# Kernel tuning notes

Hardware: AMD Instinct MI355X
Metric: run time of the kernel (lower is better)

Reference implementation:

```python
import jax, jax.numpy as jnp
import numpy as np

N_NODES = 50000
N_EDGES = 800000
IN_DIM = 512
HEADS = 4
OUT_DIM = 64


def setup_inputs() -> dict:
    key = jax.random.key(0)
    k1, k2, k3, k4 = jax.random.split(key, 4)
    x = jax.random.normal(k1, (N_NODES, IN_DIM), dtype=jnp.float32)
    edges = jax.random.randint(k2, (N_EDGES, 2), 0, N_NODES, dtype=jnp.int32)
    W = jax.random.normal(k3, (IN_DIM, HEADS * OUT_DIM), dtype=jnp.float32) * 0.05
    a = jax.random.normal(k4, (HEADS, 2 * OUT_DIM), dtype=jnp.float32) * 0.05
    bias = jnp.zeros((HEADS * OUT_DIM,), dtype=jnp.float32)
    return {"x": x, "edges": edges, "W": W, "a": a, "bias": bias}


def reference(x, edges, W, a, bias):
    num_nodes = x.shape[0]
    # project: [N, H, D]
    h = (x @ W).reshape(num_nodes, HEADS, OUT_DIM)
    src = edges[:, 0]
    dst = edges[:, 1]
    # raw attention per edge, per head: e = sum(a * concat(h_src, h_dst))
    a_src = a[:, :OUT_DIM]   # [H, D]
    a_dst = a[:, OUT_DIM:]   # [H, D]
    # precompute per-node dot-products, then gather (avoids [E,H,2D] concat)
    s_src = jnp.einsum('nhd,hd->nh', h, a_src)  # [N, H]
    s_dst = jnp.einsum('nhd,hd->nh', h, a_dst)  # [N, H]
    e = s_src[src] + s_dst[dst]                 # [E, H]
    e = jax.nn.leaky_relu(e, negative_slope=0.2)
    # softmax over edges grouped by SOURCE node (as in original code)
    max_e = jax.ops.segment_max(e, src, num_segments=num_nodes)  # [N, H]
    exp_e = jnp.exp(e - max_e[src])
    sum_exp = jax.ops.segment_sum(exp_e, src, num_segments=num_nodes)
    alpha = exp_e / (sum_exp[src] + 1e-10)       # [E, H]
    # messages aggregated at DESTINATION node
    messages = alpha[:, :, None] * h[src]        # [E, H, D]
    out = jax.ops.segment_sum(messages, dst, num_segments=num_nodes)  # [N, H, D]
    out = out.reshape(num_nodes, HEADS * OUT_DIM) + bias
    return out
```

## Files before the change

kernel.cpp:

```cpp
#include <hip/hip_runtime.h>
#include <math.h>

#define IN_DIM 512
#define NH 4
#define OD 64
#define HD 256

typedef float  floatx4 __attribute__((ext_vector_type(4)));
typedef short  shortx8 __attribute__((ext_vector_type(8)));

__device__ __forceinline__ unsigned short f2bf(float x) {
    unsigned int u = __float_as_uint(x);
    u += 0x7fffu + ((u >> 16) & 1u);
    return (unsigned short)(u >> 16);
}
__device__ __forceinline__ float bf2f(unsigned short u) {
    return __uint_as_float(((unsigned int)u) << 16);
}

__global__ void prep_kernel(const float* __restrict__ W, ushort* __restrict__ Wt,
                            int* __restrict__ head_src, int* __restrict__ head_dst,
                            int M) {
    int t = blockIdx.x * blockDim.x + threadIdx.x;
    if (t < 2 * M) head_src[t] = -1;
    if (t < 4 * M) head_dst[t] = -1;
    if (t < 256 * 64) {
        int n = t >> 6;
        int k8 = (t & 63) * 8;
        shortx8 v;
        #pragma unroll
        for (int j = 0; j < 8; ++j) v[j] = (short)f2bf(W[(size_t)(k8 + j) * HD + n]);
        *(shortx8*)&Wt[(size_t)n * IN_DIM + k8] = v;
    }
}

__global__ __launch_bounds__(256) void gemm_kernel(const float* __restrict__ x,
                                                   const ushort* __restrict__ Wt,
                                                   ushort* __restrict__ h,
                                                   const float* __restrict__ a,
                                                   float2* __restrict__ ssi,
                                                   float* __restrict__ s_dst,
                                                   int M) {
    __shared__ ushort As[64 * 64];
    __shared__ ushort Bs[256 * 64];
    const int tid = threadIdx.x;
    const int lane = tid & 63;
    const int w = tid >> 6;
    const int bm = blockIdx.x * 64;
    const int wn = w * 64;
    const int lm = lane & 15;
    const int lq = lane >> 4;
    floatx4 acc[4][4];
    #pragma unroll
    for (int i = 0; i < 4; ++i)
        #pragma unroll
        for (int j = 0; j < 4; ++j) acc[i][j] = (floatx4){0.f, 0.f, 0.f, 0.f};

    for (int k0 = 0; k0 < IN_DIM; k0 += 64) {
        #pragma unroll
        for (int j = 0; j < 2; ++j) {
            int ch = tid * 2 + j;
            int row = ch >> 3;
            int c = (ch & 7) ^ (row & 7);
            int gr = bm + row;
            shortx8 v = (shortx8){0, 0, 0, 0, 0, 0, 0, 0};
            if (gr < M) {
                const float* gp = &x[(size_t)gr * IN_DIM + k0 + c * 8];
                float4 v0 = *(const float4*)gp;
                float4 v1 = *(const float4*)(gp + 4);
                v[0] = (short)f2bf(v0.x); v[1] = (short)f2bf(v0.y);
                v[2] = (short)f2bf(v0.z); v[3] = (short)f2bf(v0.w);
                v[4] = (short)f2bf(v1.x); v[5] = (short)f2bf(v1.y);
                v[6] = (short)f2bf(v1.z); v[7] = (short)f2bf(v1.w);
            }
            *(shortx8*)&As[ch * 8] = v;
        }
        #pragma unroll
        for (int j = 0; j < 8; ++j) {
            int ch = j * 256 + tid;
            int row = ch >> 3;
            int c = (ch & 7) ^ (row & 7);
            const ushort* gp = &Wt[(size_t)row * IN_DIM + k0 + c * 8];
            __builtin_amdgcn_global_load_lds(
                (const __attribute__((address_space(1))) void*)gp,
                (__attribute__((address_space(3))) void*)&Bs[(size_t)(j * 256 + wn) * 8],
                16, 0, 0);
        }
        __syncthreads();
        #pragma unroll
        for (int kk = 0; kk < 2; ++kk) {
            shortx8 af[4], bfr[4];
            #pragma unroll
            for (int mt = 0; mt < 4; ++mt) {
                int row = mt * 16 + lm;
                int c = (kk * 4 + lq) ^ (row & 7);
                af[mt] = *(const shortx8*)&As[row * 64 + c * 8];
            }
            #pragma unroll
            for (int nt = 0; nt < 4; ++nt) {
                int row = wn + nt * 16 + lm;
                int c = (kk * 4 + lq) ^ (row & 7);
                bfr[nt] = *(const shortx8*)&Bs[row * 64 + c * 8];
            }
            #pragma unroll
            for (int mt = 0; mt < 4; ++mt)
                #pragma unroll
                for (int nt = 0; nt < 4; ++nt)
                    acc[mt][nt] = __builtin_amdgcn_mfma_f32_16x16x32_bf16(
                        af[mt], bfr[nt], acc[mt][nt], 0, 0, 0);
        }
        __syncthreads();
    }
    float as_l[4], ad_l[4];
    #pragma unroll
    for (int nt = 0; nt < 4; ++nt) {
        as_l[nt] = a[w * 2 * OD + nt * 16 + lm];
        ad_l[nt] = a[w * 2 * OD + OD + nt * 16 + lm];
    }
    #pragma unroll
    for (int mt = 0; mt < 4; ++mt)
        #pragma unroll
        for (int r = 0; r < 4; ++r) {
            float ps = 0.f, pd = 0.f;
            #pragma unroll
            for (int nt = 0; nt < 4; ++nt) {
                float v = acc[mt][nt][r];
                ps += v * as_l[nt];
                pd += v * ad_l[nt];
            }
            #pragma unroll
            for (int off = 1; off < 16; off <<= 1) {
                ps += __shfl_xor(ps, off, 64);
                pd += __shfl_xor(pd, off, 64);
            }
            int m = bm + mt * 16 + lq * 4 + r;
            if (m < M && lm == 0) {
                ssi[m * NH + w].x = ps;
                s_dst[m * NH + w] = pd;
            }
        }
    #pragma unroll
    for (int mt = 0; mt < 4; ++mt)
        #pragma unroll
        for (int r = 0; r < 4; ++r) {
            int m = bm + mt * 16 + lq * 4 + r;
            if (m < M) {
                #pragma unroll
                for (int nt = 0; nt < 4; ++nt)
                    h[(size_t)m * HD + wn + nt * 16 + lm] = f2bf(acc[mt][nt][r]);
            }
        }
}

__global__ void link_kernel(const int2* __restrict__ edges,
                            int* __restrict__ head_src, int2* __restrict__ next_src,
                            int* __restrict__ head_dst, int2* __restrict__ next_dst,
                            int E) {
    int i = blockIdx.x * blockDim.x + threadIdx.x;
    if (i >= E) return;
    int2 e = edges[i];
    int ps = atomicExch(&head_src[2 * e.x + (i & 1)], i);
    next_src[i] = make_int2(ps, e.y);
    int pd = atomicExch(&head_dst[4 * e.y + (i & 3)], i);
    next_dst[i] = make_int2(pd, e.x);
}

__global__ void src_sum_kernel(const int* __restrict__ head_src,
                               const int2* __restrict__ next_src,
                               float2* __restrict__ ssi,
                               const float* __restrict__ s_dst, int M) {
    int n = blockIdx.x * blockDim.x + threadIdx.x;
    if (n >= M) return;
    float ss0 = ssi[n * NH + 0].x, ss1 = ssi[n * NH + 1].x;
    float ss2 = ssi[n * NH + 2].x, ss3 = ssi[n * NH + 3].x;
    float4 sum = make_float4(0.f, 0.f, 0.f, 0.f);
    int e0 = head_src[2 * n], e1 = head_src[2 * n + 1];
    while (e0 != -1 || e1 != -1) {
        if (e0 != -1) {
            int2 t = next_src[e0];
            float4 sd = *(const float4*)&s_dst[t.y * NH];
            float a0 = ss0 + sd.x, a1 = ss1 + sd.y, a2 = ss2 + sd.z, a3 = ss3 + sd.w;
            a0 = a0 > 0.f ? a0 : 0.2f * a0;
            a1 = a1 > 0.f ? a1 : 0.2f * a1;
            a2 = a2 > 0.f ? a2 : 0.2f * a2;
            a3 = a3 > 0.f ? a3 : 0.2f * a3;
            sum.x += __expf(a0); sum.y += __expf(a1);
            sum.z += __expf(a2); sum.w += __expf(a3);
            e0 = t.x;
        }
        if (e1 != -1) {
            int2 t = next_src[e1];
            float4 sd = *(const float4*)&s_dst[t.y * NH];
            float a0 = ss0 + sd.x, a1 = ss1 + sd.y, a2 = ss2 + sd.z, a3 = ss3 + sd.w;
            a0 = a0 > 0.f ? a0 : 0.2f * a0;
            a1 = a1 > 0.f ? a1 : 0.2f * a1;
            a2 = a2 > 0.f ? a2 : 0.2f * a2;
            a3 = a3 > 0.f ? a3 : 0.2f * a3;
            sum.x += __expf(a0); sum.y += __expf(a1);
            sum.z += __expf(a2); sum.w += __expf(a3);
            e1 = t.x;
        }
    }
    ssi[n * NH + 0].y = 1.f / (sum.x + 1e-10f);
    ssi[n * NH + 1].y = 1.f / (sum.y + 1e-10f);
    ssi[n * NH + 2].y = 1.f / (sum.z + 1e-10f);
    ssi[n * NH + 3].y = 1.f / (sum.w + 1e-10f);
}

__global__ void gather_kernel(const int* __restrict__ head_dst,
                              const int2* __restrict__ next_dst,
                              const float2* __restrict__ ssi,
                              const float* __restrict__ s_dst,
                              const ushort* __restrict__ h,
                              const float* __restrict__ bias,
                              float* __restrict__ out, int M) {
    int lane = threadIdx.x & 63;
    int n = blockIdx.x * 4 + (threadIdx.x >> 6);
    if (n >= M) return;
    int half = lane >> 5;
    int l5 = lane & 31;
    int head = l5 >> 3;
    int c0 = l5 * 8;
    float sdst = s_dst[n * NH + head];
    floatx4 accA = {0.f, 0.f, 0.f, 0.f}, accB = {0.f, 0.f, 0.f, 0.f};
    int e0 = head_dst[4 * n + 2 * half];
    int e1 = head_dst[4 * n + 2 * half + 1];
    while (e0 != -1 || e1 != -1) {
        if (e0 != -1) {
            int2 t = next_dst[e0];
            int src = t.y;
            float2 si = ssi[src * NH + head];
            float es = si.x + sdst;
            es = es > 0.f ? es : 0.2f * es;
            float al = __expf(es) * si.y;
            shortx8 hu = *(const shortx8*)&h[(size_t)src * HD + c0];
            accA.x += al * bf2f((ushort)hu[0]); accA.y += al * bf2f((ushort)hu[1]);
            accA.z += al * bf2f((ushort)hu[2]); accA.w += al * bf2f((ushort)hu[3]);
            accB.x += al * bf2f((ushort)hu[4]); accB.y += al * bf2f((ushort)hu[5]);
            accB.z += al * bf2f((ushort)hu[6]); accB.w += al * bf2f((ushort)hu[7]);
            e0 = t.x;
        }
        if (e1 != -1) {
            int2 t = next_dst[e1];
            int src = t.y;
            float2 si = ssi[src * NH + head];
            float es = si.x + sdst;
            es = es > 0.f ? es : 0.2f * es;
            float al = __expf(es) * si.y;
            shortx8 hu = *(const shortx8*)&h[(size_t)src * HD + c0];
            accA.x += al * bf2f((ushort)hu[0]); accA.y += al * bf2f((ushort)hu[1]);
            accA.z += al * bf2f((ushort)hu[2]); accA.w += al * bf2f((ushort)hu[3]);
            accB.x += al * bf2f((ushort)hu[4]); accB.y += al * bf2f((ushort)hu[5]);
            accB.z += al * bf2f((ushort)hu[6]); accB.w += al * bf2f((ushort)hu[7]);
            e1 = t.x;
        }
    }
    accA.x += __shfl_xor(accA.x, 32, 64); accA.y += __shfl_xor(accA.y, 32, 64);
    accA.z += __shfl_xor(accA.z, 32, 64); accA.w += __shfl_xor(accA.w, 32, 64);
    accB.x += __shfl_xor(accB.x, 32, 64); accB.y += __shfl_xor(accB.y, 32, 64);
    accB.z += __shfl_xor(accB.z, 32, 64); accB.w += __shfl_xor(accB.w, 32, 64);
    if (half == 0) {
        float4 b0 = *(const float4*)&bias[c0];
        float4 b1 = *(const float4*)&bias[c0 + 4];
        float4 o0 = make_float4(accA.x + b0.x, accA.y + b0.y, accA.z + b0.z, accA.w + b0.w);
        float4 o1 = make_float4(accB.x + b1.x, accB.y + b1.y, accB.z + b1.z, accB.w + b1.w);
        *(float4*)&out[(size_t)n * HD + c0] = o0;
        *(float4*)&out[(size_t)n * HD + c0 + 4] = o1;
    }
}

extern "C" void kernel_launch(void* const* d_in, const int* in_sizes, int n_in,
                              void* d_out, int out_size, void* d_ws, size_t ws_size,
                              hipStream_t stream) {
    const float* x     = (const float*)d_in[0];
    const int2*  edges = (const int2*)d_in[1];
    const float* W     = (const float*)d_in[2];
    const float* a     = (const float*)d_in[3];
    const float* bias  = (const float*)d_in[4];
    float* out = (float*)d_out;
    const int M = in_sizes[0] / IN_DIM;
    const int E = in_sizes[1] / 2;

    char* p = (char*)d_ws;
    ushort* hB       = (ushort*)p; p += (size_t)M * HD * sizeof(ushort);
    ushort* Wt       = (ushort*)p; p += (size_t)HD * IN_DIM * sizeof(ushort);
    float*  s_dst    = (float*)p;  p += (size_t)M * NH * sizeof(float);
    float2* ssi      = (float2*)p; p += (size_t)M * NH * sizeof(float2);
    int*    head_src = (int*)p;    p += (size_t)2 * M * sizeof(int);
    int*    head_dst = (int*)p;    p += (size_t)4 * M * sizeof(int);
    int2*   next_src = (int2*)p;   p += (size_t)E * sizeof(int2);
    int2*   next_dst = (int2*)p;   p += (size_t)E * sizeof(int2);

    prep_kernel<<<(4 * M + 255) / 256, 256, 0, stream>>>(W, Wt, head_src, head_dst, M);
    gemm_kernel<<<(M + 63) / 64, 256, 0, stream>>>(x, Wt, hB, a, ssi, s_dst, M);
    link_kernel<<<(E + 255) / 256, 256, 0, stream>>>(edges, head_src, next_src,
                                                     head_dst, next_dst, E);
    src_sum_kernel<<<(M + 255) / 256, 256, 0, stream>>>(head_src, next_src, ssi, s_dst, M);
    gather_kernel<<<(M + 3) / 4, 256, 0, stream>>>(head_dst, next_dst, ssi, s_dst,
                                                   hB, bias, out, M);
}
```

Baseline: 367.1 us.

## Replace linked-list edge traversal with CSR build and atomic softmax sums

Replaces the per-node linked lists (atomicExch heads plus next pointers) with a CSR layout keyed by destination, built from a degree count, a single-block scan and an atomic scatter. The source-side softmax denominators are now accumulated per edge with float atomics instead of a separate per-node list walk. The gather walks contiguous CSR ranges two edges at a time instead of chasing dependent pointers. This trades serial pointer-chasing latency for an extra scan launch, a single-block scan, and float atomic contention, whose summation order becomes nondeterministic.

```diff
diff --git a/kernel.cpp b/kernel.cpp
--- a/kernel.cpp
+++ b/kernel.cpp
@@ -19,11 +19,11 @@
 }
 
 __global__ void prep_kernel(const float* __restrict__ W, ushort* __restrict__ Wt,
-                            int* __restrict__ head_src, int* __restrict__ head_dst,
+                            int* __restrict__ deg, float* __restrict__ sumexp,
                             int M) {
     int t = blockIdx.x * blockDim.x + threadIdx.x;
-    if (t < 2 * M) head_src[t] = -1;
-    if (t < 4 * M) head_dst[t] = -1;
+    if (t < M) deg[t] = 0;
+    if (t < 4 * M) sumexp[t] = 0.f;
     if (t < 256 * 64) {
         int n = t >> 6;
         int k8 = (t & 63) * 8;
@@ -38,7 +38,7 @@
                                                    const ushort* __restrict__ Wt,
                                                    ushort* __restrict__ h,
                                                    const float* __restrict__ a,
-                                                   float2* __restrict__ ssi,
+                                                   float* __restrict__ s_src,
                                                    float* __restrict__ s_dst,
                                                    int M) {
     __shared__ ushort As[64 * 64];
@@ -135,7 +135,7 @@
             }
             int m = bm + mt * 16 + lq * 4 + r;
             if (m < M && lm == 0) {
-                ssi[m * NH + w].x = ps;
+                s_src[m * NH + w] = ps;
                 s_dst[m * NH + w] = pd;
             }
         }
@@ -152,68 +152,75 @@
         }
 }
 
-__global__ void link_kernel(const int2* __restrict__ edges,
-                            int* __restrict__ head_src, int2* __restrict__ next_src,
-                            int* __restrict__ head_dst, int2* __restrict__ next_dst,
-                            int E) {
+__global__ void count_sum_kernel(const int2* __restrict__ edges,
+                                 const float* __restrict__ s_src,
+                                 const float* __restrict__ s_dst,
+                                 int* __restrict__ deg,
+                                 float* __restrict__ sumexp, int E) {
     int i = blockIdx.x * blockDim.x + threadIdx.x;
     if (i >= E) return;
     int2 e = edges[i];
-    int ps = atomicExch(&head_src[2 * e.x + (i & 1)], i);
-    next_src[i] = make_int2(ps, e.y);
-    int pd = atomicExch(&head_dst[4 * e.y + (i & 3)], i);
-    next_dst[i] = make_int2(pd, e.x);
-}
-
-__global__ void src_sum_kernel(const int* __restrict__ head_src,
-                               const int2* __restrict__ next_src,
-                               float2* __restrict__ ssi,
-                               const float* __restrict__ s_dst, int M) {
-    int n = blockIdx.x * blockDim.x + threadIdx.x;
-    if (n >= M) return;
-    float ss0 = ssi[n * NH + 0].x, ss1 = ssi[n * NH + 1].x;
-    float ss2 = ssi[n * NH + 2].x, ss3 = ssi[n * NH + 3].x;
-    float4 sum = make_float4(0.f, 0.f, 0.f, 0.f);
-    int e0 = head_src[2 * n], e1 = head_src[2 * n + 1];
-    while (e0 != -1 || e1 != -1) {
-        if (e0 != -1) {
-            int2 t = next_src[e0];
-            float4 sd = *(const float4*)&s_dst[t.y * NH];
-            float a0 = ss0 + sd.x, a1 = ss1 + sd.y, a2 = ss2 + sd.z, a3 = ss3 + sd.w;
-            a0 = a0 > 0.f ? a0 : 0.2f * a0;
-            a1 = a1 > 0.f ? a1 : 0.2f * a1;
-            a2 = a2 > 0.f ? a2 : 0.2f * a2;
-            a3 = a3 > 0.f ? a3 : 0.2f * a3;
-            sum.x += __expf(a0); sum.y += __expf(a1);
-            sum.z += __expf(a2); sum.w += __expf(a3);
-            e0 = t.x;
-        }
-        if (e1 != -1) {
-            int2 t = next_src[e1];
-            float4 sd = *(const float4*)&s_dst[t.y * NH];
-            float a0 = ss0 + sd.x, a1 = ss1 + sd.y, a2 = ss2 + sd.z, a3 = ss3 + sd.w;
-            a0 = a0 > 0.f ? a0 : 0.2f * a0;
-            a1 = a1 > 0.f ? a1 : 0.2f * a1;
-            a2 = a2 > 0.f ? a2 : 0.2f * a2;
-            a3 = a3 > 0.f ? a3 : 0.2f * a3;
-            sum.x += __expf(a0); sum.y += __expf(a1);
-            sum.z += __expf(a2); sum.w += __expf(a3);
-            e1 = t.x;
-        }
-    }
-    ssi[n * NH + 0].y = 1.f / (sum.x + 1e-10f);
-    ssi[n * NH + 1].y = 1.f / (sum.y + 1e-10f);
-    ssi[n * NH + 2].y = 1.f / (sum.z + 1e-10f);
-    ssi[n * NH + 3].y = 1.f / (sum.w + 1e-10f);
-}
-
-__global__ void gather_kernel(const int* __restrict__ head_dst,
-                              const int2* __restrict__ next_dst,
-                              const float2* __restrict__ ssi,
-                              const float* __restrict__ s_dst,
-                              const ushort* __restrict__ h,
-                              const float* __restrict__ bias,
-                              float* __restrict__ out, int M) {
+    atomicAdd(&deg[e.y], 1);
+    float4 ss = *(const float4*)&s_src[(size_t)e.x * NH];
+    float4 sd = *(const float4*)&s_dst[(size_t)e.y * NH];
+    float a0 = ss.x + sd.x, a1 = ss.y + sd.y, a2 = ss.z + sd.z, a3 = ss.w + sd.w;
+    a0 = a0 > 0.f ? a0 : 0.2f * a0;
+    a1 = a1 > 0.f ? a1 : 0.2f * a1;
+    a2 = a2 > 0.f ? a2 : 0.2f * a2;
+    a3 = a3 > 0.f ? a3 : 0.2f * a3;
+    atomicAdd(&sumexp[(size_t)e.x * NH + 0], __expf(a0));
+    atomicAdd(&sumexp[(size_t)e.x * NH + 1], __expf(a1));
+    atomicAdd(&sumexp[(size_t)e.x * NH + 2], __expf(a2));
+    atomicAdd(&sumexp[(size_t)e.x * NH + 3], __expf(a3));
+}
+
+__global__ __launch_bounds__(1024) void scan_kernel(const int* __restrict__ deg,
+                                                    int* __restrict__ ptr,
+                                                    int* __restrict__ cursor, int M) {
+    __shared__ int sdata[1024];
+    const int t = threadIdx.x;
+    const int C = (M + 1023) >> 10;
+    const int base = t * C;
+    int sum = 0;
+    for (int j = 0; j < C; ++j) {
+        int i = base + j;
+        if (i < M) sum += deg[i];
+    }
+    sdata[t] = sum;
+    __syncthreads();
+    for (int off = 1; off < 1024; off <<= 1) {
+        int v = (t >= off) ? sdata[t - off] : 0;
+        __syncthreads();
+        sdata[t] += v;
+        __syncthreads();
+    }
+    int run = sdata[t] - sum;
+    for (int j = 0; j < C; ++j) {
+        int i = base + j;
+        if (i < M) {
+            ptr[i] = run;
+            cursor[i] = run;
+            run += deg[i];
+        }
+    }
+    if (t == 1023) ptr[M] = run;
+}
+
+__global__ void scatter_kernel(const int2* __restrict__ edges,
+                               int* __restrict__ cursor,
+                               int* __restrict__ csr_src, int E) {
+    int i = blockIdx.x * blockDim.x + threadIdx.x;
+    if (i >= E) return;
+    int2 e = edges[i];
+    int pos = atomicAdd(&cursor[e.y], 1);
+    csr_src[pos] = e.x;
+}
+
+__global__ __launch_bounds__(256) void gather_kernel(
+        const int* __restrict__ ptr, const int* __restrict__ csr_src,
+        const float* __restrict__ s_src, const float* __restrict__ sumexp,
+        const float* __restrict__ s_dst, const ushort* __restrict__ h,
+        const float* __restrict__ bias, float* __restrict__ out, int M) {
     int lane = threadIdx.x & 63;
     int n = blockIdx.x * 4 + (threadIdx.x >> 6);
     if (n >= M) return;
@@ -223,38 +230,44 @@
     int c0 = l5 * 8;
     float sdst = s_dst[n * NH + head];
     floatx4 accA = {0.f, 0.f, 0.f, 0.f}, accB = {0.f, 0.f, 0.f, 0.f};
-    int e0 = head_dst[4 * n + 2 * half];
-    int e1 = head_dst[4 * n + 2 * half + 1];
-    while (e0 != -1 || e1 != -1) {
-        if (e0 != -1) {
-            int2 t = next_dst[e0];
-            int src = t.y;
-            float2 si = ssi[src * NH + head];
-            float es = si.x + sdst;
-            es = es > 0.f ? es : 0.2f * es;
-            float al = __expf(es) * si.y;
-            shortx8 hu = *(const shortx8*)&h[(size_t)src * HD + c0];
-            accA.x += al * bf2f((ushort)hu[0]); accA.y += al * bf2f((ushort)hu[1]);
-            accA.z += al * bf2f((ushort)hu[2]); accA.w += al * bf2f((ushort)hu[3]);
-            accB.x += al * bf2f((ushort)hu[4]); accB.y += al * bf2f((ushort)hu[5]);
-            accB.z += al * bf2f((ushort)hu[6]); accB.w += al * bf2f((ushort)hu[7]);
-            e0 = t.x;
-        }
-        if (e1 != -1) {
-            int2 t = next_dst[e1];
-            int src = t.y;
-            float2 si = ssi[src * NH + head];
-            float es = si.x + sdst;
-            es = es > 0.f ? es : 0.2f * es;
-            float al = __expf(es) * si.y;
-            shortx8 hu = *(const shortx8*)&h[(size_t)src * HD + c0];
-            accA.x += al * bf2f((ushort)hu[0]); accA.y += al * bf2f((ushort)hu[1]);
-            accA.z += al * bf2f((ushort)hu[2]); accA.w += al * bf2f((ushort)hu[3]);
-            accB.x += al * bf2f((ushort)hu[4]); accB.y += al * bf2f((ushort)hu[5]);
-            accB.z += al * bf2f((ushort)hu[6]); accB.w += al * bf2f((ushort)hu[7]);
-            e1 = t.x;
-        }
-    }
+    int beg = ptr[n], end = ptr[n + 1];
+    int e = beg + half;
+
+#define GAT_EDGE(SS, SM, HU) do {                                              \
+        float es_ = (SS) + sdst;                                               \
+        es_ = es_ > 0.f ? es_ : 0.2f * es_;                                    \
+        float al_ = __expf(es_) * __builtin_amdgcn_rcpf((SM) + 1e-10f);        \
+        accA.x += al_ * bf2f((ushort)(HU)[0]);                                 \
+        accA.y += al_ * bf2f((ushort)(HU)[1]);                                 \
+        accA.z += al_ * bf2f((ushort)(HU)[2]);                                 \
+        accA.w += al_ * bf2f((ushort)(HU)[3]);                                 \
+        accB.x += al_ * bf2f((ushort)(HU)[4]);                                 \
+        accB.y += al_ * bf2f((ushort)(HU)[5]);                                 \
+        accB.z += al_ * bf2f((ushort)(HU)[6]);                                 \
+        accB.w += al_ * bf2f((ushort)(HU)[7]);                                 \
+    } while (0)
+
+    for (; e + 2 < end; e += 4) {
+        int s0 = csr_src[e];
+        int s1 = csr_src[e + 2];
+        float ss0 = s_src[(size_t)s0 * NH + head];
+        float sm0 = sumexp[(size_t)s0 * NH + head];
+        float ss1 = s_src[(size_t)s1 * NH + head];
+        float sm1 = sumexp[(size_t)s1 * NH + head];
+        shortx8 h0 = *(const shortx8*)&h[(size_t)s0 * HD + c0];
+        shortx8 h1 = *(const shortx8*)&h[(size_t)s1 * HD + c0];
+        GAT_EDGE(ss0, sm0, h0);
+        GAT_EDGE(ss1, sm1, h1);
+    }
+    if (e < end) {
+        int s0 = csr_src[e];
+        float ss0 = s_src[(size_t)s0 * NH + head];
+        float sm0 = sumexp[(size_t)s0 * NH + head];
+        shortx8 h0 = *(const shortx8*)&h[(size_t)s0 * HD + c0];
+        GAT_EDGE(ss0, sm0, h0);
+    }
+#undef GAT_EDGE
+
     accA.x += __shfl_xor(accA.x, 32, 64); accA.y += __shfl_xor(accA.y, 32, 64);
     accA.z += __shfl_xor(accA.z, 32, 64); accA.w += __shfl_xor(accA.w, 32, 64);
     accB.x += __shfl_xor(accB.x, 32, 64); accB.y += __shfl_xor(accB.y, 32, 64);
@@ -282,20 +295,22 @@
     const int E = in_sizes[1] / 2;
 
     char* p = (char*)d_ws;
-    ushort* hB       = (ushort*)p; p += (size_t)M * HD * sizeof(ushort);
-    ushort* Wt       = (ushort*)p; p += (size_t)HD * IN_DIM * sizeof(ushort);
-    float*  s_dst    = (float*)p;  p += (size_t)M * NH * sizeof(float);
-    float2* ssi      = (float2*)p; p += (size_t)M * NH * sizeof(float2);
-    int*    head_src = (int*)p;    p += (size_t)2 * M * sizeof(int);
-    int*    head_dst = (int*)p;    p += (size_t)4 * M * sizeof(int);
-    int2*   next_src = (int2*)p;   p += (size_t)E * sizeof(int2);
-    int2*   next_dst = (int2*)p;   p += (size_t)E * sizeof(int2);
-
-    prep_kernel<<<(4 * M + 255) / 256, 256, 0, stream>>>(W, Wt, head_src, head_dst, M);
-    gemm_kernel<<<(M + 63) / 64, 256, 0, stream>>>(x, Wt, hB, a, ssi, s_dst, M);
-    link_kernel<<<(E + 255) / 256, 256, 0, stream>>>(edges, head_src, next_src,
-                                                     head_dst, next_dst, E);
-    src_sum_kernel<<<(M + 255) / 256, 256, 0, stream>>>(head_src, next_src, ssi, s_dst, M);
-    gather_kernel<<<(M + 3) / 4, 256, 0, stream>>>(head_dst, next_dst, ssi, s_dst,
-                                                   hB, bias, out, M);
-}
+    ushort* hB      = (ushort*)p; p += (size_t)M * HD * sizeof(ushort);
+    ushort* Wt      = (ushort*)p; p += (size_t)HD * IN_DIM * sizeof(ushort);
+    float*  s_src   = (float*)p;  p += (size_t)M * NH * sizeof(float);
+    float*  s_dst   = (float*)p;  p += (size_t)M * NH * sizeof(float);
+    float*  sumexp  = (float*)p;  p += (size_t)M * NH * sizeof(float);
+    int*    deg     = (int*)p;    p += (size_t)M * sizeof(int);
+    int*    ptr     = (int*)p;    p += ((size_t)M + 4) * sizeof(int);
+    int*    cursor  = (int*)p;    p += (size_t)M * sizeof(int);
+    int*    csr_src = (int*)p;    p += (size_t)E * sizeof(int);
+
+    prep_kernel<<<(4 * M + 255) / 256, 256, 0, stream>>>(W, Wt, deg, sumexp, M);
+    gemm_kernel<<<(M + 63) / 64, 256, 0, stream>>>(x, Wt, hB, a, s_src, s_dst, M);
+    count_sum_kernel<<<(E + 255) / 256, 256, 0, stream>>>(edges, s_src, s_dst,
+                                                          deg, sumexp, E);
+    scan_kernel<<<1, 1024, 0, stream>>>(deg, ptr, cursor, M);
+    scatter_kernel<<<(E + 255) / 256, 256, 0, stream>>>(edges, cursor, csr_src, E);
+    gather_kernel<<<(M + 3) / 4, 256, 0, stream>>>(ptr, csr_src, s_src, sumexp,
+                                                   s_dst, hB, bias, out, M);
+}
```

New measurement: 629.7 us. 1.72x slower.

## Split adjacency lists into more chains and walk them in parallel

Applied to the files above, without the earlier changes.

Each source node's edge list is split into 16 linked chains instead of 2, and each destination node's into 8 instead of 4. src_sum now uses one wavefront per node, with 16 chain slots times 4 heads handled by separate lanes and combined by shuffle reduction. gather now walks four chains per half-wave at once and issues the loads before the compute, so memory-level parallelism is higher. This shortens the serial pointer-chasing latency chains, at the cost of larger head arrays to initialise and more idle lanes on short chains.

```diff
diff --git a/kernel.cpp b/kernel.cpp
--- a/kernel.cpp
+++ b/kernel.cpp
@@ -22,8 +22,8 @@
                             int* __restrict__ head_src, int* __restrict__ head_dst,
                             int M) {
     int t = blockIdx.x * blockDim.x + threadIdx.x;
-    if (t < 2 * M) head_src[t] = -1;
-    if (t < 4 * M) head_dst[t] = -1;
+    if (t < 16 * M) head_src[t] = -1;
+    if (t < 8 * M) head_dst[t] = -1;
     if (t < 256 * 64) {
         int n = t >> 6;
         int k8 = (t & 63) * 8;
@@ -159,55 +159,40 @@
     int i = blockIdx.x * blockDim.x + threadIdx.x;
     if (i >= E) return;
     int2 e = edges[i];
-    int ps = atomicExch(&head_src[2 * e.x + (i & 1)], i);
+    int ps = atomicExch(&head_src[16 * e.x + (i & 15)], i);
     next_src[i] = make_int2(ps, e.y);
-    int pd = atomicExch(&head_dst[4 * e.y + (i & 3)], i);
+    int pd = atomicExch(&head_dst[8 * e.y + (i & 7)], i);
     next_dst[i] = make_int2(pd, e.x);
 }
 
-__global__ void src_sum_kernel(const int* __restrict__ head_src,
-                               const int2* __restrict__ next_src,
-                               float2* __restrict__ ssi,
-                               const float* __restrict__ s_dst, int M) {
-    int n = blockIdx.x * blockDim.x + threadIdx.x;
+__global__ __launch_bounds__(256) void src_sum_kernel(const int* __restrict__ head_src,
+                                                      const int2* __restrict__ next_src,
+                                                      float2* __restrict__ ssi,
+                                                      const float* __restrict__ s_dst, int M) {
+    int lane = threadIdx.x & 63;
+    int n = blockIdx.x * 4 + (threadIdx.x >> 6);
     if (n >= M) return;
-    float ss0 = ssi[n * NH + 0].x, ss1 = ssi[n * NH + 1].x;
-    float ss2 = ssi[n * NH + 2].x, ss3 = ssi[n * NH + 3].x;
-    float4 sum = make_float4(0.f, 0.f, 0.f, 0.f);
-    int e0 = head_src[2 * n], e1 = head_src[2 * n + 1];
-    while (e0 != -1 || e1 != -1) {
-        if (e0 != -1) {
-            int2 t = next_src[e0];
-            float4 sd = *(const float4*)&s_dst[t.y * NH];
-            float a0 = ss0 + sd.x, a1 = ss1 + sd.y, a2 = ss2 + sd.z, a3 = ss3 + sd.w;
-            a0 = a0 > 0.f ? a0 : 0.2f * a0;
-            a1 = a1 > 0.f ? a1 : 0.2f * a1;
-            a2 = a2 > 0.f ? a2 : 0.2f * a2;
-            a3 = a3 > 0.f ? a3 : 0.2f * a3;
-            sum.x += __expf(a0); sum.y += __expf(a1);
-            sum.z += __expf(a2); sum.w += __expf(a3);
-            e0 = t.x;
-        }
-        if (e1 != -1) {
-            int2 t = next_src[e1];
-            float4 sd = *(const float4*)&s_dst[t.y * NH];
-            float a0 = ss0 + sd.x, a1 = ss1 + sd.y, a2 = ss2 + sd.z, a3 = ss3 + sd.w;
-            a0 = a0 > 0.f ? a0 : 0.2f * a0;
-            a1 = a1 > 0.f ? a1 : 0.2f * a1;
-            a2 = a2 > 0.f ? a2 : 0.2f * a2;
-            a3 = a3 > 0.f ? a3 : 0.2f * a3;
-            sum.x += __expf(a0); sum.y += __expf(a1);
-            sum.z += __expf(a2); sum.w += __expf(a3);
-            e1 = t.x;
-        }
-    }
-    ssi[n * NH + 0].y = 1.f / (sum.x + 1e-10f);
-    ssi[n * NH + 1].y = 1.f / (sum.y + 1e-10f);
-    ssi[n * NH + 2].y = 1.f / (sum.z + 1e-10f);
-    ssi[n * NH + 3].y = 1.f / (sum.w + 1e-10f);
-}
-
-__global__ void gather_kernel(const int* __restrict__ head_dst,
+    int slot = lane >> 2;
+    int hd = lane & 3;
+    float ss = ssi[n * NH + hd].x;
+    float sum = 0.f;
+    int e = head_src[16 * n + slot];
+    while (e != -1) {
+        int2 t = next_src[e];
+        float sd = s_dst[t.y * NH + hd];
+        float a0 = ss + sd;
+        a0 = a0 > 0.f ? a0 : 0.2f * a0;
+        sum += __expf(a0);
+        e = t.x;
+    }
+    sum += __shfl_xor(sum, 4, 64);
+    sum += __shfl_xor(sum, 8, 64);
+    sum += __shfl_xor(sum, 16, 64);
+    sum += __shfl_xor(sum, 32, 64);
+    if (lane < 4) ssi[n * NH + lane].y = 1.f / (sum + 1e-10f);
+}
+
+__global__ __launch_bounds__(256) void gather_kernel(const int* __restrict__ head_dst,
                               const int2* __restrict__ next_dst,
                               const float2* __restrict__ ssi,
                               const float* __restrict__ s_dst,
@@ -223,38 +208,47 @@
     int c0 = l5 * 8;
     float sdst = s_dst[n * NH + head];
     floatx4 accA = {0.f, 0.f, 0.f, 0.f}, accB = {0.f, 0.f, 0.f, 0.f};
-    int e0 = head_dst[4 * n + 2 * half];
-    int e1 = head_dst[4 * n + 2 * half + 1];
-    while (e0 != -1 || e1 != -1) {
-        if (e0 != -1) {
-            int2 t = next_dst[e0];
-            int src = t.y;
-            float2 si = ssi[src * NH + head];
-            float es = si.x + sdst;
-            es = es > 0.f ? es : 0.2f * es;
-            float al = __expf(es) * si.y;
-            shortx8 hu = *(const shortx8*)&h[(size_t)src * HD + c0];
-            accA.x += al * bf2f((ushort)hu[0]); accA.y += al * bf2f((ushort)hu[1]);
-            accA.z += al * bf2f((ushort)hu[2]); accA.w += al * bf2f((ushort)hu[3]);
-            accB.x += al * bf2f((ushort)hu[4]); accB.y += al * bf2f((ushort)hu[5]);
-            accB.z += al * bf2f((ushort)hu[6]); accB.w += al * bf2f((ushort)hu[7]);
-            e0 = t.x;
-        }
-        if (e1 != -1) {
-            int2 t = next_dst[e1];
-            int src = t.y;
-            float2 si = ssi[src * NH + head];
-            float es = si.x + sdst;
-            es = es > 0.f ? es : 0.2f * es;
-            float al = __expf(es) * si.y;
-            shortx8 hu = *(const shortx8*)&h[(size_t)src * HD + c0];
-            accA.x += al * bf2f((ushort)hu[0]); accA.y += al * bf2f((ushort)hu[1]);
-            accA.z += al * bf2f((ushort)hu[2]); accA.w += al * bf2f((ushort)hu[3]);
-            accB.x += al * bf2f((ushort)hu[4]); accB.y += al * bf2f((ushort)hu[5]);
-            accB.z += al * bf2f((ushort)hu[6]); accB.w += al * bf2f((ushort)hu[7]);
-            e1 = t.x;
-        }
-    }
+    int e0 = head_dst[8 * n + 4 * half + 0];
+    int e1 = head_dst[8 * n + 4 * half + 1];
+    int e2 = head_dst[8 * n + 4 * half + 2];
+    int e3 = head_dst[8 * n + 4 * half + 3];
+
+    while (e0 != -1 || e1 != -1 || e2 != -1 || e3 != -1) {
+        bool b0 = e0 != -1, b1 = e1 != -1, b2 = e2 != -1, b3 = e3 != -1;
+        int2 t0, t1, t2, t3;
+        if (b0) t0 = next_dst[e0];
+        if (b1) t1 = next_dst[e1];
+        if (b2) t2 = next_dst[e2];
+        if (b3) t3 = next_dst[e3];
+        float2 si0, si1, si2, si3;
+        shortx8 h0, h1, h2, h3;
+        if (b0) { si0 = ssi[(size_t)t0.y * NH + head]; h0 = *(const shortx8*)&h[(size_t)t0.y * HD + c0]; }
+        if (b1) { si1 = ssi[(size_t)t1.y * NH + head]; h1 = *(const shortx8*)&h[(size_t)t1.y * HD + c0]; }
+        if (b2) { si2 = ssi[(size_t)t2.y * NH + head]; h2 = *(const shortx8*)&h[(size_t)t2.y * HD + c0]; }
+        if (b3) { si3 = ssi[(size_t)t3.y * NH + head]; h3 = *(const shortx8*)&h[(size_t)t3.y * HD + c0]; }
+#define GAT_EDGE(B, SI, HU, EV, TV) do {                                       \
+        if (B) {                                                               \
+            float es_ = (SI).x + sdst;                                         \
+            es_ = es_ > 0.f ? es_ : 0.2f * es_;                                \
+            float al_ = __expf(es_) * (SI).y;                                  \
+            accA.x += al_ * bf2f((ushort)(HU)[0]);                             \
+            accA.y += al_ * bf2f((ushort)(HU)[1]);                             \
+            accA.z += al_ * bf2f((ushort)(HU)[2]);                             \
+            accA.w += al_ * bf2f((ushort)(HU)[3]);                             \
+            accB.x += al_ * bf2f((ushort)(HU)[4]);                             \
+            accB.y += al_ * bf2f((ushort)(HU)[5]);                             \
+            accB.z += al_ * bf2f((ushort)(HU)[6]);                             \
+            accB.w += al_ * bf2f((ushort)(HU)[7]);                             \
+            EV = (TV).x;                                                       \
+        }                                                                      \
+    } while (0)
+        GAT_EDGE(b0, si0, h0, e0, t0);
+        GAT_EDGE(b1, si1, h1, e1, t1);
+        GAT_EDGE(b2, si2, h2, e2, t2);
+        GAT_EDGE(b3, si3, h3, e3, t3);
+#undef GAT_EDGE
+    }
+
     accA.x += __shfl_xor(accA.x, 32, 64); accA.y += __shfl_xor(accA.y, 32, 64);
     accA.z += __shfl_xor(accA.z, 32, 64); accA.w += __shfl_xor(accA.w, 32, 64);
     accB.x += __shfl_xor(accB.x, 32, 64); accB.y += __shfl_xor(accB.y, 32, 64);
@@ -286,16 +280,16 @@
     ushort* Wt       = (ushort*)p; p += (size_t)HD * IN_DIM * sizeof(ushort);
     float*  s_dst    = (float*)p;  p += (size_t)M * NH * sizeof(float);
     float2* ssi      = (float2*)p; p += (size_t)M * NH * sizeof(float2);
-    int*    head_src = (int*)p;    p += (size_t)2 * M * sizeof(int);
-    int*    head_dst = (int*)p;    p += (size_t)4 * M * sizeof(int);
+    int*    head_src = (int*)p;    p += (size_t)16 * M * sizeof(int);
+    int*    head_dst = (int*)p;    p += (size_t)8 * M * sizeof(int);
     int2*   next_src = (int2*)p;   p += (size_t)E * sizeof(int2);
     int2*   next_dst = (int2*)p;   p += (size_t)E * sizeof(int2);
 
-    prep_kernel<<<(4 * M + 255) / 256, 256, 0, stream>>>(W, Wt, head_src, head_dst, M);
+    prep_kernel<<<(16 * M + 255) / 256, 256, 0, stream>>>(W, Wt, head_src, head_dst, M);
     gemm_kernel<<<(M + 63) / 64, 256, 0, stream>>>(x, Wt, hB, a, ssi, s_dst, M);
     link_kernel<<<(E + 255) / 256, 256, 0, stream>>>(edges, head_src, next_src,
                                                      head_dst, next_dst, E);
-    src_sum_kernel<<<(M + 255) / 256, 256, 0, stream>>>(head_src, next_src, ssi, s_dst, M);
+    src_sum_kernel<<<(M + 3) / 4, 256, 0, stream>>>(head_src, next_src, ssi, s_dst, M);
     gather_kernel<<<(M + 3) / 4, 256, 0, stream>>>(head_dst, next_dst, ssi, s_dst,
                                                    hB, bias, out, M);
 }
```

New measurement: 361.9 us. About the same (-1.4%).
